# Kernel optimization log

Measured on AMD Instinct MI355X. Metric: run time of the kernel, lower is better.

Reference implementation:

```python
import jax, jax.numpy as jnp
import numpy as np
import itertools

N_BITS = 64   # data_info['n']
K_MAX = 3     # data_info['k']
BATCH = 8192


def _build_table(n, k):
    # All 0/1 vectors of length n with at most k ones, ordered by popcount then lexicographic
    rows = [np.zeros((1, n), dtype=np.int32)]
    for i in range(1, k + 1):
        idxs = np.array(list(itertools.combinations(range(n), i)), dtype=np.int64)  # (C(n,i), i)
        t = np.zeros((idxs.shape[0], n), dtype=np.int32)
        t[np.arange(idxs.shape[0])[:, None], idxs] = 1
        rows.append(t)
    return np.concatenate(rows, axis=0)  # (total_case, n)


def setup_inputs() -> dict:
    key = jax.random.key(0)
    table_np = _build_table(N_BITS, K_MAX)
    total_case = table_np.shape[0]  # 43745 for n=64, k=3
    k1, k2 = jax.random.split(key)
    # x must exactly match a table row (original code's .nonzero()[0] assumes a match exists)
    sel = jax.random.randint(k1, (BATCH,), 0, total_case)
    table = jnp.asarray(table_np)
    x = table[sel]  # (BATCH, n) int32, each row has <= k ones
    W = jax.random.normal(k2, (total_case,), dtype=jnp.float32)
    return {"x": x, "table": table, "W": W}


def reference(x, table, W):
    # Original per-sample loop: idx_i = first row r with sum(table[r] ^ x_i) == 0.
    # For 0/1 vectors, sum(a ^ b) = sum(a) + sum(b) - 2 * (a . b), so the whole
    # batch reduces to one GEMM + an equality test + argmax (first True).
    xf = x.astype(jnp.float32)
    tf = table.astype(jnp.float32)
    xs = jnp.sum(xf, axis=1)          # (B,)
    ts = jnp.sum(tf, axis=1)          # (T,)
    dot = xf @ tf.T                   # (B, T)
    mismatch = xs[:, None] + ts[None, :] - 2.0 * dot  # (B, T) popcount of XOR
    idx = jnp.argmax(mismatch == 0.0, axis=1)         # first exact match per row
    logw = jnp.log(jax.nn.softmax(W))                 # matches torch: log(softmax(W))
    return logw[idx]                                  # (B,)
```

## Files before the change

kernel.cpp:

```cpp
#include <hip/hip_runtime.h>

__global__ void partial_exp_kernel(const float* __restrict__ W, int T,
                                   float* __restrict__ partials) {
    __shared__ float red[4];
    const int tid  = threadIdx.x;
    const int lane = tid & 63;
    const int wave = tid >> 6;
    float s = 0.0f;
    for (int i = blockIdx.x * blockDim.x + tid; i < T; i += gridDim.x * blockDim.x)
        s += expf(W[i]);
    for (int off = 32; off > 0; off >>= 1) s += __shfl_down(s, off, 64);
    if (lane == 0) red[wave] = s;
    __syncthreads();
    if (tid == 0)
        partials[blockIdx.x] = red[0] + red[1] + red[2] + red[3];
}

__global__ void rank_kernel(const int* __restrict__ x,
                            const float* __restrict__ W,
                            const float* __restrict__ partials,
                            float* __restrict__ out, int batch) {
    const int lane = threadIdx.x & 63;
    const int row  = (int)((blockIdx.x * blockDim.x + threadIdx.x) >> 6);
    if (row >= batch) return;

    float p = (lane < 32) ? partials[lane] : 0.0f;
    for (int off = 32; off > 0; off >>= 1) p += __shfl_down(p, off, 64);

    const int v = x[row * 64 + lane];
    const unsigned long long mask = __ballot(v != 0);
    if (lane == 0) {
        const int m = __popcll(mask);
        int idx;
        if (m == 0) {
            idx = 0;
        } else {
            unsigned long long t = mask;
            const int a = __builtin_ctzll(t); t &= t - 1;
            if (m == 1) {
                idx = 1 + a;
            } else {
                const int b = __builtin_ctzll(t); t &= t - 1;
                if (m == 2) {
                    idx = 65 + ((4032 - (63 - a) * (64 - a)) >> 1) + (b - a - 1);
                } else {
                    const int c = __builtin_ctzll(t);
                    const int s1 = 41664 - ((64 - a) * (63 - a) * (62 - a)) / 6;
                    const int s2 = ((62 - a) * (63 - a) - (63 - b) * (64 - b)) >> 1;
                    idx = 2081 + s1 + s2 + (c - b - 1);
                }
            }
        }
        out[row] = W[idx] - logf(p);
    }
}

extern "C" void kernel_launch(void* const* d_in, const int* in_sizes, int n_in,
                              void* d_out, int out_size, void* d_ws, size_t ws_size,
                              hipStream_t stream) {
    const int*   x = (const int*)d_in[0];
    const float* W = (const float*)d_in[2];
    float* out      = (float*)d_out;
    float* partials = (float*)d_ws;

    const int T = in_sizes[2];
    const int B = in_sizes[0] / 64;

    partial_exp_kernel<<<32, 256, 0, stream>>>(W, T, partials);

    const int threads = 256;
    const int rows_per_block = threads / 64;
    const int blocks = (B + rows_per_block - 1) / rows_per_block;
    rank_kernel<<<blocks, threads, 0, stream>>>(x, W, partials, out, B);
}
```

Measured before the change: 67.64 us.

## Fuse softmax normalizer into rank kernel with per-block redundant reduction

Merges the two kernels into one launch: every block recomputes the full sum of exp(W) with float4 loads and fast exp/log intrinsics, then handles 16 rows (4 per wave) for index ranking. This removes the second launch, the inter-kernel dependency and the workspace round trip. In exchange each of the ~512 blocks rereads all of W and redoes the exponentials, which multiplies L2 traffic and ALU work. It also uses less precise __expf/__logf.

Result: slower. 75.32 us (+11.4%).

```diff
diff --git a/kernel.cpp b/kernel.cpp
--- a/kernel.cpp
+++ b/kernel.cpp
@@ -1,57 +1,71 @@
 #include <hip/hip_runtime.h>
 
-__global__ void partial_exp_kernel(const float* __restrict__ W, int T,
-                                   float* __restrict__ partials) {
+__global__ __launch_bounds__(256) void fused_rank_kernel(
+        const int* __restrict__ x,
+        const float* __restrict__ W, int T,
+        float* __restrict__ out, int batch) {
     __shared__ float red[4];
+    __shared__ float s_lse;
     const int tid  = threadIdx.x;
     const int lane = tid & 63;
     const int wave = tid >> 6;
+
     float s = 0.0f;
-    for (int i = blockIdx.x * blockDim.x + tid; i < T; i += gridDim.x * blockDim.x)
-        s += expf(W[i]);
+    const int T4 = T >> 2;
+    const float4* __restrict__ W4 = (const float4*)W;
+    for (int i = tid; i < T4; i += 256) {
+        const float4 v = W4[i];
+        s += __expf(v.x) + __expf(v.y) + __expf(v.z) + __expf(v.w);
+    }
+    for (int i = (T4 << 2) + tid; i < T; i += 256)
+        s += __expf(W[i]);
+    #pragma unroll
     for (int off = 32; off > 0; off >>= 1) s += __shfl_down(s, off, 64);
     if (lane == 0) red[wave] = s;
     __syncthreads();
-    if (tid == 0)
-        partials[blockIdx.x] = red[0] + red[1] + red[2] + red[3];
-}
+    if (tid == 0) s_lse = __logf(red[0] + red[1] + red[2] + red[3]);
+    __syncthreads();
+    const float lse = s_lse;
 
-__global__ void rank_kernel(const int* __restrict__ x,
-                            const float* __restrict__ W,
-                            const float* __restrict__ partials,
-                            float* __restrict__ out, int batch) {
-    const int lane = threadIdx.x & 63;
-    const int row  = (int)((blockIdx.x * blockDim.x + threadIdx.x) >> 6);
-    if (row >= batch) return;
+    const int row0 = blockIdx.x * 16 + wave * 4;
+    int v0 = 0, v1 = 0, v2 = 0, v3 = 0;
+    if (row0 + 0 < batch) v0 = x[(size_t)(row0 + 0) * 64 + lane];
+    if (row0 + 1 < batch) v1 = x[(size_t)(row0 + 1) * 64 + lane];
+    if (row0 + 2 < batch) v2 = x[(size_t)(row0 + 2) * 64 + lane];
+    if (row0 + 3 < batch) v3 = x[(size_t)(row0 + 3) * 64 + lane];
+    const unsigned long long m0 = __ballot(v0 != 0);
+    const unsigned long long m1 = __ballot(v1 != 0);
+    const unsigned long long m2 = __ballot(v2 != 0);
+    const unsigned long long m3 = __ballot(v3 != 0);
 
-    float p = (lane < 32) ? partials[lane] : 0.0f;
-    for (int off = 32; off > 0; off >>= 1) p += __shfl_down(p, off, 64);
-
-    const int v = x[row * 64 + lane];
-    const unsigned long long mask = __ballot(v != 0);
-    if (lane == 0) {
-        const int m = __popcll(mask);
-        int idx;
-        if (m == 0) {
-            idx = 0;
-        } else {
-            unsigned long long t = mask;
-            const int a = __builtin_ctzll(t); t &= t - 1;
-            if (m == 1) {
-                idx = 1 + a;
+    if (lane < 4) {
+        const int row = row0 + lane;
+        if (row < batch) {
+            const unsigned long long mask =
+                (lane == 0) ? m0 : (lane == 1) ? m1 : (lane == 2) ? m2 : m3;
+            const int m = __popcll(mask);
+            int idx;
+            if (m == 0) {
+                idx = 0;
             } else {
-                const int b = __builtin_ctzll(t); t &= t - 1;
-                if (m == 2) {
-                    idx = 65 + ((4032 - (63 - a) * (64 - a)) >> 1) + (b - a - 1);
+                unsigned long long t = mask;
+                const int a = __builtin_ctzll(t); t &= t - 1;
+                if (m == 1) {
+                    idx = 1 + a;
                 } else {
-                    const int c = __builtin_ctzll(t);
-                    const int s1 = 41664 - ((64 - a) * (63 - a) * (62 - a)) / 6;
-                    const int s2 = ((62 - a) * (63 - a) - (63 - b) * (64 - b)) >> 1;
-                    idx = 2081 + s1 + s2 + (c - b - 1);
+                    const int b = __builtin_ctzll(t); t &= t - 1;
+                    if (m == 2) {
+                        idx = 65 + ((4032 - (63 - a) * (64 - a)) >> 1) + (b - a - 1);
+                    } else {
+                        const int c = __builtin_ctzll(t);
+                        const int s1 = 41664 - ((64 - a) * (63 - a) * (62 - a)) / 6;
+                        const int s2 = ((62 - a) * (63 - a) - (63 - b) * (64 - b)) >> 1;
+                        idx = 2081 + s1 + s2 + (c - b - 1);
+                    }
                 }
             }
+            out[row] = W[idx] - lse;
         }
-        out[row] = W[idx] - logf(p);
     }
 }
 
@@ -60,16 +74,12 @@
                               hipStream_t stream) {
     const int*   x = (const int*)d_in[0];
     const float* W = (const float*)d_in[2];
-    float* out      = (float*)d_out;
-    float* partials = (float*)d_ws;
+    float* out     = (float*)d_out;
+    (void)d_ws; (void)ws_size;
 
     const int T = in_sizes[2];
     const int B = in_sizes[0] / 64;
 
-    partial_exp_kernel<<<32, 256, 0, stream>>>(W, T, partials);
-
-    const int threads = 256;
-    const int rows_per_block = threads / 64;
-    const int blocks = (B + rows_per_block - 1) / rows_per_block;
-    rank_kernel<<<blocks, threads, 0, stream>>>(x, W, partials, out, B);
+    const int blocks = (B + 15) / 16;
+    fused_rank_kernel<<<blocks, 256, 0, stream>>>(x, W, T, out, B);
 }
```
